# Kernel tuning notes

Measured on AMD Instinct MI355X. Metric: run time of the kernel, lower is better.

Reference implementation:

```python
import jax, jax.numpy as jnp
import numpy as np


def _patch_desc(x, patch_size):
    # x: (n, c, h, w). Replicate-pad by patch_size//2 and gather all
    # patch_size*patch_size shifted views -> (n, c*p*p, h*w) descriptors.
    n, c, h, w = x.shape
    step = patch_size // 2
    y = jnp.pad(x, ((0, 0), (0, 0), (step, step), (step, step)), mode='edge')
    feats = [y[:, :, i:i + h, j:j + w]
             for i in range(patch_size) for j in range(patch_size)]
    d = jnp.stack(feats, axis=2)            # (n, c, p*p, h, w)
    return d.reshape(n, c * patch_size * patch_size, h * w)


def setup_inputs() -> dict:
    key = jax.random.key(0)
    k1, k2 = jax.random.split(key)
    n, c, h, w = 4, 16, 64, 64
    s = jax.random.normal(k1, (n, c, h, w), dtype=jnp.float32)
    t = jax.random.normal(k2, (n, c, h, w), dtype=jnp.float32)
    return {"s": s, "t": t, "patch_size": 3}


def reference(s, t, patch_size):
    n, c, h, w = s.shape
    q = _patch_desc(s, patch_size)          # (n, d, hw) source queries
    p = _patch_desc(t, patch_size)          # (n, d, hw) target points
    # Squared-L2 nearest neighbor per source patch (exact version of FLANN kNN)
    qn = jnp.sum(q * q, axis=1)             # (n, hw)
    pn = jnp.sum(p * p, axis=1)             # (n, hw)
    cross = jnp.einsum('ndi,ndj->nij', q, p)  # (n, hw_q, hw_t)
    d2 = qn[:, :, None] - 2.0 * cross + pn[:, None, :]
    idx = jnp.argmin(d2, axis=2)            # (n, hw) flat target index
    nnd = jnp.min(d2, axis=2)               # (n, hw) squared distance
    idy = idx // w
    idx_x = idx % w
    nnf = jnp.stack([idy.reshape(n, h, w), idx_x.reshape(n, h, w)], axis=1)
    nnd = nnd.reshape(n, 1, h, w)
    return nnf.astype(jnp.int32), nnd
```

## Files before the change

kernel.cpp:

```cpp
#include <hip/hip_runtime.h>


#define N_  4
#define C_  16
#define H_  64
#define W_  64
#define HW_ 4096
#define KK_ 18
#define SPLITS_M 4
#define KKSTRIDE 512

#define SPLITS_V 4
#define TILES_PER_SPLIT_V 4

typedef _Float16 f16;
typedef _Float16 f16x8 __attribute__((ext_vector_type(8)));
typedef float    f32x4 __attribute__((ext_vector_type(4)));
typedef float    f32x16 __attribute__((ext_vector_type(16)));

__device__ __forceinline__ int iclamp(int v, int lo, int hi) {
    return v < lo ? lo : (v > hi ? hi : v);
}

__device__ __forceinline__ void async_ld16(const void* g, void* l) {
    __builtin_amdgcn_global_load_lds(
        (const __attribute__((address_space(1))) unsigned int*)g,
        (__attribute__((address_space(3))) unsigned int*)l, 16, 0, 0);
}

__global__ __launch_bounds__(256)
void build_desc_norms_kernel(const float* __restrict__ s,
                             const float* __restrict__ t,
                             f16* __restrict__ Qh, f16* __restrict__ Ql,
                             f16* __restrict__ Ph, f16* __restrict__ Pl,
                             float* __restrict__ pn,
                             float* __restrict__ qn) {
    const int y0  = blockIdx.x;
    const int n   = blockIdx.y;
    const int src = blockIdx.z;
    const float* img = (src ? s : t) + n * (C_ * HW_);
    f16* Dh = src ? Qh : Ph;
    f16* Dl = src ? Ql : Pl;
    float* nrm = src ? qn : pn;

    __shared__ float imgS[3][C_][W_];
    __shared__ float nS[4][W_];
    const int tid = threadIdx.x;
    #pragma unroll
    for (int k = 0; k < 12; ++k) {
        const int idx = tid + k * 256;
        const int x = idx & 63, c = (idx >> 6) & 15, r = idx >> 10;
        const int gy = iclamp(y0 + r - 1, 0, H_ - 1);
        imgS[r][c][x] = img[c * HW_ + gy * W_ + x];
    }
    __syncthreads();

    const int q = tid >> 6, x = tid & 63;
    const int pix = y0 * W_ + x;
    float nacc = 0.f;
    #pragma unroll
    for (int u = 0; u < 5; ++u) {
        const int kk = q * 5 + u;
        if (kk < KK_) {
            f16x8 hv, lv;
            const int d  = kk >> 1;
            const int c0 = (kk & 1) * 8;
            const int dy = (d * 11) >> 5;
            const int dx = d - dy * 3;
            const int xs = iclamp(x + dx - 1, 0, W_ - 1);
            #pragma unroll
            for (int cc = 0; cc < 8; ++cc) {
                const float v = imgS[dy][c0 + cc][xs];
                const f16 h = (f16)v;
                hv[cc] = h;
                lv[cc] = (f16)(v - (float)h);
                nacc += v * v;
            }
            const size_t off = ((size_t)(n * KK_ + kk) * HW_ + pix) * 8;
            *(f16x8*)&Dh[off] = hv;
            *(f16x8*)&Dl[off] = lv;
        }
    }
    nS[q][x] = nacc;
    __syncthreads();
    if (tid < W_)
        nrm[n * HW_ + pix] = nS[0][tid] + nS[1][tid] + nS[2][tid] + nS[3][tid];
}

__global__ __launch_bounds__(256, 2)
void mfma_nn_kernel(const f16* __restrict__ Qh, const f16* __restrict__ Ql,
                    const f16* __restrict__ Ph, const f16* __restrict__ Pl,
                    const float* __restrict__ pn_g,
                    unsigned long long* __restrict__ partial) {
    const int bid   = blockIdx.x;
    const int split = bid & 3;
    const int n     = (bid >> 2) & 3;
    const int iblk  = bid >> 4;
    const int tid  = threadIdx.x;
    const int wave = tid >> 6, lane = tid & 63;
    const int col  = lane & 31;
    const int half = lane >> 5;
    const int irow0 = iblk * 128 + wave * 32;

    __shared__ f16 Bbuf[4][KK_ * KKSTRIDE];
    __shared__ float pnS[1024];

    f16x8 Ah[9], Al[9];
    #pragma unroll
    for (int c = 0; c < 9; ++c) {
        const size_t off = ((size_t)(n * KK_ + 2 * c + half) * HW_ +
                            irow0 + col) * 8;
        Ah[c] = *(const f16x8*)(Qh + off);
        Al[c] = *(const f16x8*)(Ql + off);
    }

    const int jsplit0 = split * 1024;
    #pragma unroll
    for (int k = 0; k < 4; ++k)
        pnS[tid + k * 256] = pn_g[n * HW_ + jsplit0 + tid + k * 256];

    float    bd[16];
    unsigned bj[16];
    #pragma unroll
    for (int r = 0; r < 16; ++r) { bd[r] = -3.0e38f; bj[r] = 0u; }

    const int stile = wave >> 1;
    const int skk0  = (wave & 1) * 9;
    const f16* sbase = half ? Pl : Ph;

    #define STAGE(PAIR, T0)                                                   \
        {   _Pragma("unroll")                                                 \
            for (int u = 0; u < 9; ++u) {                                     \
                const int kk = skk0 + u;                                      \
                const f16* g = sbase + ((size_t)(n * KK_ + kk) * HW_ +        \
                                        jsplit0 + ((T0) + stile) * 32 +       \
                                        col) * 8;                             \
                async_ld16(g, (void*)&Bbuf[(PAIR) * 2 + stile]                \
                                          [kk * KKSTRIDE + lane * 8]);        \
            }                                                                 \
        }

    #define BAR()                                                             \
        {   asm volatile("s_waitcnt vmcnt(0)" ::: "memory");                  \
            asm volatile("s_barrier" ::: "memory");                           \
        }

    #define COMPUTE2(PAIR, T0)                                                \
        {   const int j0 = (T0) * 32 + col;                                   \
            const float pnv0 = -0.5f * pnS[j0];                               \
            const float pnv1 = -0.5f * pnS[j0 + 32];                          \
            f32x16 C0, C1;                                                    \
            _Pragma("unroll")                                                 \
            for (int r = 0; r < 16; ++r) { C0[r] = pnv0; C1[r] = pnv1; }      \
            __builtin_amdgcn_s_setprio(1);                                    \
            _Pragma("unroll")                                                 \
            for (int c = 0; c < 9; ++c) {                                     \
                const int kb = (2 * c + half) * KKSTRIDE + col * 8;           \
                const f16x8 bh0 = *(const f16x8*)&Bbuf[(PAIR) * 2][kb];       \
                const f16x8 bl0 = *(const f16x8*)&Bbuf[(PAIR) * 2][kb + 256]; \
                const f16x8 bh1 = *(const f16x8*)&Bbuf[(PAIR) * 2 + 1][kb];   \
                const f16x8 bl1 = *(const f16x8*)&Bbuf[(PAIR) * 2 + 1]        \
                                                      [kb + 256];             \
                C0 = __builtin_amdgcn_mfma_f32_32x32x16_f16(                  \
                    Ah[c], bh0, C0, 0, 0, 0);                                 \
                C1 = __builtin_amdgcn_mfma_f32_32x32x16_f16(                  \
                    Ah[c], bh1, C1, 0, 0, 0);                                 \
                C0 = __builtin_amdgcn_mfma_f32_32x32x16_f16(                  \
                    Al[c], bh0, C0, 0, 0, 0);                                 \
                C1 = __builtin_amdgcn_mfma_f32_32x32x16_f16(                  \
                    Al[c], bh1, C1, 0, 0, 0);                                 \
                C0 = __builtin_amdgcn_mfma_f32_32x32x16_f16(                  \
                    Ah[c], bl0, C0, 0, 0, 0);                                 \
                C1 = __builtin_amdgcn_mfma_f32_32x32x16_f16(                  \
                    Ah[c], bl1, C1, 0, 0, 0);                                 \
            }                                                                 \
            __builtin_amdgcn_s_setprio(0);                                    \
            _Pragma("unroll")                                                 \
            for (int r = 0; r < 16; ++r) {                                    \
                if (C0[r] > bd[r]) { bd[r] = C0[r]; bj[r] = (unsigned)j0; }   \
                if (C1[r] > bd[r]) { bd[r] = C1[r];                           \
                                     bj[r] = (unsigned)(j0 + 32); }           \
            }                                                                 \
        }

    STAGE(0, 0)
    asm volatile("s_waitcnt vmcnt(0)" ::: "memory");
    __syncthreads();

    STAGE(1, 2)  COMPUTE2(0, 0)
    for (int gg = 0; gg < 6; ++gg) {
        const int t4 = gg * 4;
        BAR()  STAGE(0, t4 + 4)  COMPUTE2(1, t4 + 2)
        BAR()  STAGE(1, t4 + 6)  COMPUTE2(0, t4 + 4)
    }
    BAR()  STAGE(0, 28)  COMPUTE2(1, 26)
    BAR()  STAGE(1, 30)  COMPUTE2(0, 28)
    BAR()               COMPUTE2(1, 30)
    #undef STAGE
    #undef BAR
    #undef COMPUTE2

    #pragma unroll
    for (int r = 0; r < 16; ++r) {
        float    d = bd[r];
        unsigned j = (unsigned)jsplit0 + bj[r];
        #pragma unroll
        for (int off = 1; off < 32; off <<= 1) {
            const float    od = __shfl_xor(d, off, 64);
            const unsigned oj = __shfl_xor(j, off, 64);
            const bool take = (od > d) || (od == d && oj < j);
            d = take ? od : d;
            j = take ? oj : j;
        }
        if (col == 0) {
            const int i = irow0 + (r & 3) + 8 * (r >> 2) + 4 * half;
            partial[(size_t)(split * N_ + n) * HW_ + i] =
                ((unsigned long long)j << 32) |
                (unsigned long long)__float_as_uint(-2.f * d);
        }
    }
}

__global__ __launch_bounds__(256)
void finalize_mfma_kernel(const unsigned long long* __restrict__ partial,
                          const float* __restrict__ qn_g,
                          float* __restrict__ out) {
    const int id  = blockIdx.x * 256 + threadIdx.x;
    const int n   = id >> 12;
    const int pix = id & 4095;
    float    bd = 3.0e38f;
    unsigned bj = 0u;
    #pragma unroll
    for (int sp = 0; sp < SPLITS_M; ++sp) {
        const unsigned long long v = partial[(size_t)(sp * N_ + n) * HW_ + pix];
        const float    d = __uint_as_float((unsigned)(v & 0xffffffffull));
        const unsigned j = (unsigned)(v >> 32);
        const bool take = (d < bd) || (d == bd && j < bj);
        bd = take ? d : bd;
        bj = take ? j : bj;
    }
    out[n * 2 * HW_ + pix]            = (float)(bj >> 6);
    out[n * 2 * HW_ + HW_ + pix]      = (float)(bj & 63);
    out[N_ * 2 * HW_ + n * HW_ + pix] = bd + qn_g[n * HW_ + pix];
}

__global__ __launch_bounds__(256)
void prep_norms_kernel(const float* __restrict__ s,
                       const float* __restrict__ t,
                       float* __restrict__ pn,
                       float* __restrict__ qn) {
    const int gid   = blockIdx.x * 256 + threadIdx.x;
    const int which = gid >> 14;
    const int id    = gid & 16383;
    const int n     = id >> 12;
    const int pix   = id & 4095;
    const int y = pix >> 6, x = pix & 63;
    const float* base = (which ? s : t) + n * (C_ * HW_);
    float acc = 0.f;
    for (int c = 0; c < C_; ++c) {
        const float* bc = base + c * HW_;
        #pragma unroll
        for (int dy = 0; dy < 3; ++dy) {
            const float* br = bc + iclamp(y + dy - 1, 0, H_ - 1) * W_;
            #pragma unroll
            for (int dx = 0; dx < 3; ++dx) {
                float v = br[iclamp(x + dx - 1, 0, W_ - 1)];
                acc += v * v;
            }
        }
    }
    (which ? qn : pn)[id] = acc;
}

__global__ __launch_bounds__(256)
void patchmatch_main_kernel(const float* __restrict__ s,
                            const float* __restrict__ t,
                            const float* __restrict__ pn_g,
                            const float* __restrict__ qn_g,
                            unsigned long long* __restrict__ partial) {
    const int yq    = blockIdx.x;
    const int n     = blockIdx.y;
    const int split = blockIdx.z;
    const int tid  = threadIdx.x;
    const int tx   = tid & 15;
    const int ty   = tid >> 4;
    const int i0   = ty * 4;
    const int jrow = tx >> 2;
    const int jx0  = (tx & 3) * 16;

    __shared__ float qS[C_][3][68];
    __shared__ float tS[C_][6][68];
    __shared__ float qnS[W_];

    const float* sb = s + n * (C_ * HW_);
    const float* tb = t + n * (C_ * HW_);

    #pragma unroll
    for (int k = 0; k < 3; ++k) {
        const int id = tid + k * 256;
        const int sg = id & 15;
        const int c  = (id >> 4) & 15;
        const int r  = id >> 8;
        const int gr = iclamp(yq + r - 1, 0, H_ - 1);
        const float4 v = *(const float4*)&sb[c * HW_ + gr * W_ + sg * 4];
        float* dst = &qS[c][r][1 + sg * 4];
        dst[0] = v.x; dst[1] = v.y; dst[2] = v.z; dst[3] = v.w;
    }
    if (tid < 48) {
        const int c  = tid & 15;
        const int r  = tid >> 4;
        const int gr = iclamp(yq + r - 1, 0, H_ - 1);
        qS[c][r][0]  = sb[c * HW_ + gr * W_];
        qS[c][r][65] = sb[c * HW_ + gr * W_ + 63];
    }
    if (tid < W_) qnS[tid] = qn_g[n * HW_ + yq * W_ + tid];

    unsigned long long best[4] = {~0ull, ~0ull, ~0ull, ~0ull};

    for (int ytl = 0; ytl < TILES_PER_SPLIT_V; ++ytl) {
        const int yt = split * TILES_PER_SPLIT_V + ytl;
        __syncthreads();
        #pragma unroll
        for (int k = 0; k < 6; ++k) {
            const int id = tid + k * 256;
            const int sg = id & 15;
            const int c  = (id >> 4) & 15;
            const int r  = id >> 8;
            const int gr = iclamp(4 * yt + r - 1, 0, H_ - 1);
            const float4 v = *(const float4*)&tb[c * HW_ + gr * W_ + sg * 4];
            float* dst = &tS[c][r][1 + sg * 4];
            dst[0] = v.x; dst[1] = v.y; dst[2] = v.z; dst[3] = v.w;
        }
        if (tid < 96) {
            const int c  = tid & 15;
            const int r  = tid >> 4;
            const int gr = iclamp(4 * yt + r - 1, 0, H_ - 1);
            tS[c][r][0]  = tb[c * HW_ + gr * W_];
            tS[c][r][65] = tb[c * HW_ + gr * W_ + 63];
        }
        __syncthreads();

        float acc[4][16];
        #pragma unroll
        for (int a = 0; a < 4; ++a)
            #pragma unroll
            for (int b = 0; b < 16; ++b) acc[a][b] = 0.f;

        for (int c = 0; c < C_; ++c) {
            #pragma unroll
            for (int dy = 0; dy < 3; ++dy) {
                float qv[6], tv[18];
                *(float4*)&qv[0] = *(const float4*)&qS[c][dy][i0];
                *(float2*)&qv[4] = *(const float2*)&qS[c][dy][i0 + 4];
                const float* trow = &tS[c][jrow + dy][jx0];
                *(float4*)&tv[0]  = *(const float4*)&trow[0];
                *(float4*)&tv[4]  = *(const float4*)&trow[4];
                *(float4*)&tv[8]  = *(const float4*)&trow[8];
                *(float4*)&tv[12] = *(const float4*)&trow[12];
                *(float2*)&tv[16] = *(const float2*)&trow[16];
                #pragma unroll
                for (int dx = 0; dx < 3; ++dx)
                    #pragma unroll
                    for (int a = 0; a < 4; ++a)
                        #pragma unroll
                        for (int b = 0; b < 16; ++b)
                            acc[a][b] += qv[a + dx] * tv[b + dx];
            }
        }

        const int jbase = yt * 256 + jrow * W_ + jx0;
        float pnv[16];
        const float* png = &pn_g[n * HW_ + jbase];
        *(float4*)&pnv[0]  = *(const float4*)&png[0];
        *(float4*)&pnv[4]  = *(const float4*)&png[4];
        *(float4*)&pnv[8]  = *(const float4*)&png[8];
        *(float4*)&pnv[12] = *(const float4*)&png[12];
        #pragma unroll
        for (int a = 0; a < 4; ++a) {
            const float qn = qnS[i0 + a];
            #pragma unroll
            for (int b = 0; b < 16; ++b) {
                const float d2 = qn + pnv[b] - 2.f * acc[a][b];
                unsigned long long cand =
                    ((unsigned long long)__float_as_uint(d2) << 32) |
                    (unsigned)(jbase + b);
                best[a] = cand < best[a] ? cand : best[a];
            }
        }
    }

    #pragma unroll
    for (int a = 0; a < 4; ++a) {
        unsigned long long v = best[a];
        #pragma unroll
        for (int mm = 8; mm >= 1; mm >>= 1) {
            unsigned long long o = __shfl_xor(v, mm, 64);
            v = o < v ? o : v;
        }
        best[a] = v;
    }
    if (tx == 0) {
        #pragma unroll
        for (int a = 0; a < 4; ++a)
            partial[((split * N_ + n) * HW_) + yq * W_ + i0 + a] = best[a];
    }
}

__global__ __launch_bounds__(256)
void finalize_kernel(const unsigned long long* __restrict__ partial,
                     float* __restrict__ out) {
    const int id  = blockIdx.x * 256 + threadIdx.x;
    const int n   = id >> 12;
    const int pix = id & 4095;
    unsigned long long best = ~0ull;
    #pragma unroll
    for (int sp = 0; sp < SPLITS_V; ++sp) {
        unsigned long long v = partial[(sp * N_ + n) * HW_ + pix];
        best = v < best ? v : best;
    }
    const unsigned j = (unsigned)(best & 0xffffffffu);
    const float d2 = __uint_as_float((unsigned)(best >> 32));
    out[n * 2 * HW_ + pix]            = (float)(j >> 6);
    out[n * 2 * HW_ + HW_ + pix]      = (float)(j & 63);
    out[N_ * 2 * HW_ + n * HW_ + pix] = d2;
}

__global__ __launch_bounds__(256)
void patchmatch_mono_kernel(const float* __restrict__ s,
                            const float* __restrict__ t,
                            float* __restrict__ out) {
    const int yq  = blockIdx.x;
    const int n   = blockIdx.y;
    const int tid = threadIdx.x;
    const int tx  = tid & 15;
    const int ty  = tid >> 4;
    const int i0  = ty * 4;
    const int jrow = tx >> 3;
    const int jx0  = (tx & 7) * 8;

    __shared__ float qS[C_][3][68];
    __shared__ float tS[C_][4][68];
    __shared__ float pnS[HW_];
    __shared__ float qnS[W_];

    const float* sb = s + n * (C_ * HW_);
    const float* tb = t + n * (C_ * HW_);

    for (int jj = tid; jj < HW_; jj += 256) {
        const int y = jj >> 6, x = jj & 63;
        float acc = 0.f;
        for (int c = 0; c < C_; ++c) {
            const float* tc = tb + c * HW_;
            #pragma unroll
            for (int dy = 0; dy < 3; ++dy) {
                const float* tr = tc + iclamp(y + dy - 1, 0, H_ - 1) * W_;
                #pragma unroll
                for (int dx = 0; dx < 3; ++dx) {
                    float v = tr[iclamp(x + dx - 1, 0, W_ - 1)];
                    acc += v * v;
                }
            }
        }
        pnS[jj] = acc;
    }
    for (int idx = tid; idx < C_ * 3 * 66; idx += 256) {
        const int c   = idx / (3 * 66);
        const int rem = idx - c * (3 * 66);
        const int rr  = rem / 66;
        const int xi  = rem - rr * 66;
        qS[c][rr][xi] = sb[c * HW_ + iclamp(yq + rr - 1, 0, H_ - 1) * W_ +
                           iclamp(xi - 1, 0, W_ - 1)];
    }
    __syncthreads();
    if (tid < W_) {
        float acc = 0.f;
        for (int c = 0; c < C_; ++c)
            #pragma unroll
            for (int dy = 0; dy < 3; ++dy)
                #pragma unroll
                for (int dx = 0; dx < 3; ++dx) {
                    float v = qS[c][dy][tid + dx];
                    acc += v * v;
                }
        qnS[tid] = acc;
    }

    unsigned long long best[4] = {~0ull, ~0ull, ~0ull, ~0ull};
    for (int yt = 0; yt < 32; ++yt) {
        __syncthreads();
        for (int idx = tid; idx < C_ * 4 * 66; idx += 256) {
            const int c   = idx / (4 * 66);
            const int rem = idx - c * (4 * 66);
            const int rr  = rem / 66;
            const int xi  = rem - rr * 66;
            tS[c][rr][xi] = tb[c * HW_ + iclamp(2 * yt + rr - 1, 0, H_ - 1) * W_ +
                               iclamp(xi - 1, 0, W_ - 1)];
        }
        __syncthreads();

        float acc[4][8];
        #pragma unroll
        for (int a = 0; a < 4; ++a)
            #pragma unroll
            for (int b = 0; b < 8; ++b) acc[a][b] = 0.f;

        for (int c = 0; c < C_; ++c) {
            #pragma unroll
            for (int dy = 0; dy < 3; ++dy) {
                float qv[8], tv[12];
                *(float4*)&qv[0] = *(const float4*)&qS[c][dy][i0];
                *(float4*)&qv[4] = *(const float4*)&qS[c][dy][i0 + 4];
                const float* trow = &tS[c][jrow + dy][jx0];
                *(float4*)&tv[0] = *(const float4*)&trow[0];
                *(float4*)&tv[4] = *(const float4*)&trow[4];
                *(float4*)&tv[8] = *(const float4*)&trow[8];
                #pragma unroll
                for (int dx = 0; dx < 3; ++dx)
                    #pragma unroll
                    for (int a = 0; a < 4; ++a)
                        #pragma unroll
                        for (int b = 0; b < 8; ++b)
                            acc[a][b] += qv[a + dx] * tv[b + dx];
            }
        }
        const int rbase = (2 * yt + jrow) * W_ + jx0;
        #pragma unroll
        for (int a = 0; a < 4; ++a) {
            const float qn = qnS[i0 + a];
            #pragma unroll
            for (int b = 0; b < 8; ++b) {
                const int j = rbase + b;
                const float d2 = qn + pnS[j] - 2.f * acc[a][b];
                unsigned long long cand =
                    ((unsigned long long)__float_as_uint(d2) << 32) | (unsigned)j;
                best[a] = cand < best[a] ? cand : best[a];
            }
        }
    }
    #pragma unroll
    for (int a = 0; a < 4; ++a) {
        unsigned long long v = best[a];
        #pragma unroll
        for (int mm = 8; mm >= 1; mm >>= 1) {
            unsigned long long o = __shfl_xor(v, mm, 64);
            v = o < v ? o : v;
        }
        best[a] = v;
    }
    if (tx == 0) {
        #pragma unroll
        for (int a = 0; a < 4; ++a) {
            const int x = i0 + a;
            const unsigned j = (unsigned)(best[a] & 0xffffffffu);
            const float d2 = __uint_as_float((unsigned)(best[a] >> 32));
            const int pix = yq * W_ + x;
            out[n * 2 * HW_ + pix]            = (float)(j >> 6);
            out[n * 2 * HW_ + HW_ + pix]      = (float)(j & 63);
            out[N_ * 2 * HW_ + n * HW_ + pix] = d2;
        }
    }
}

extern "C" void kernel_launch(void* const* d_in, const int* in_sizes, int n_in,
                              void* d_out, int out_size, void* d_ws, size_t ws_size,
                              hipStream_t stream) {
    const float* s = (const float*)d_in[0];
    const float* t = (const float*)d_in[1];
    float* out = (float*)d_out;

    const size_t norm_b  = (size_t)N_ * HW_ * 4;
    const size_t part_b  = (size_t)SPLITS_M * N_ * HW_ * 8;
    const size_t desc_b  = (size_t)N_ * HW_ * KK_ * 8 * 2;
    const size_t need_m  = 2 * norm_b + part_b + 4 * desc_b;

    if (ws_size >= need_m) {
        char* w = (char*)d_ws;
        float* pn = (float*)w;                       w += norm_b;
        float* qn = (float*)w;                       w += norm_b;
        unsigned long long* partial = (unsigned long long*)w; w += part_b;
        f16* Qh = (f16*)w;  w += desc_b;
        f16* Ql = (f16*)w;  w += desc_b;
        f16* Ph = (f16*)w;  w += desc_b;
        f16* Pl = (f16*)w;

        build_desc_norms_kernel<<<dim3(64, N_, 2), 256, 0, stream>>>(
            s, t, Qh, Ql, Ph, Pl, pn, qn);
        mfma_nn_kernel<<<512, 256, 0, stream>>>(Qh, Ql, Ph, Pl, pn, partial);
        finalize_mfma_kernel<<<64, 256, 0, stream>>>(partial, qn, out);
        return;
    }

    const size_t need_v = 2 * norm_b + (size_t)SPLITS_V * N_ * HW_ * 8;
    if (ws_size >= need_v) {
        float* pn = (float*)d_ws;
        float* qn = pn + N_ * HW_;
        unsigned long long* partial =
            (unsigned long long*)((char*)d_ws + 2 * norm_b);
        prep_norms_kernel<<<128, 256, 0, stream>>>(s, t, pn, qn);
        dim3 grid(H_, N_, SPLITS_V);
        patchmatch_main_kernel<<<grid, 256, 0, stream>>>(s, t, pn, qn, partial);
        finalize_kernel<<<64, 256, 0, stream>>>(partial, out);
        return;
    }

    dim3 grid(H_, N_);
    patchmatch_mono_kernel<<<grid, 256, 0, stream>>>(s, t, out);
}
```

Baseline: 124.4 us.

## Load B operand directly from global memory instead of LDS double-buffering

Removes the async global-to-LDS staging pipeline with its double buffer and per-step barriers. Each wave now reads its B fragments (high and low halves of the target descriptors) straight from global memory into registers inside the MFMA loop, unrolled by two. This frees a large shared-memory footprint and the barrier stalls. The cost is that the four waves of a block each re-read the same B tiles from global/L2, and global-load latency now sits directly in the MFMA loop with no explicit prefetch.

```diff
diff --git a/kernel.cpp b/kernel.cpp
--- a/kernel.cpp
+++ b/kernel.cpp
@@ -8,8 +8,6 @@
 #define HW_ 4096
 #define KK_ 18
 #define SPLITS_M 4
-#define KKSTRIDE 512
-
 #define SPLITS_V 4
 #define TILES_PER_SPLIT_V 4
 
@@ -20,12 +18,6 @@
 
 __device__ __forceinline__ int iclamp(int v, int lo, int hi) {
     return v < lo ? lo : (v > hi ? hi : v);
-}
-
-__device__ __forceinline__ void async_ld16(const void* g, void* l) {
-    __builtin_amdgcn_global_load_lds(
-        (const __attribute__((address_space(1))) unsigned int*)g,
-        (__attribute__((address_space(3))) unsigned int*)l, 16, 0, 0);
 }
 
 __global__ __launch_bounds__(256)
@@ -102,7 +94,6 @@
     const int half = lane >> 5;
     const int irow0 = iblk * 128 + wave * 32;
 
-    __shared__ f16 Bbuf[4][KK_ * KKSTRIDE];
     __shared__ float pnS[1024];
 
     f16x8 Ah[9], Al[9];
@@ -118,87 +109,48 @@
     #pragma unroll
     for (int k = 0; k < 4; ++k)
         pnS[tid + k * 256] = pn_g[n * HW_ + jsplit0 + tid + k * 256];
+    __syncthreads();
 
     float    bd[16];
     unsigned bj[16];
     #pragma unroll
     for (int r = 0; r < 16; ++r) { bd[r] = -3.0e38f; bj[r] = 0u; }
 
-    const int stile = wave >> 1;
-    const int skk0  = (wave & 1) * 9;
-    const f16* sbase = half ? Pl : Ph;
-
-    #define STAGE(PAIR, T0)                                                   \
-        {   _Pragma("unroll")                                                 \
-            for (int u = 0; u < 9; ++u) {                                     \
-                const int kk = skk0 + u;                                      \
-                const f16* g = sbase + ((size_t)(n * KK_ + kk) * HW_ +        \
-                                        jsplit0 + ((T0) + stile) * 32 +       \
-                                        col) * 8;                             \
-                async_ld16(g, (void*)&Bbuf[(PAIR) * 2 + stile]                \
-                                          [kk * KKSTRIDE + lane * 8]);        \
-            }                                                                 \
-        }
-
-    #define BAR()                                                             \
-        {   asm volatile("s_waitcnt vmcnt(0)" ::: "memory");                  \
-            asm volatile("s_barrier" ::: "memory");                           \
-        }
-
-    #define COMPUTE2(PAIR, T0)                                                \
-        {   const int j0 = (T0) * 32 + col;                                   \
-            const float pnv0 = -0.5f * pnS[j0];                               \
-            const float pnv1 = -0.5f * pnS[j0 + 32];                          \
-            f32x16 C0, C1;                                                    \
-            _Pragma("unroll")                                                 \
-            for (int r = 0; r < 16; ++r) { C0[r] = pnv0; C1[r] = pnv1; }      \
-            __builtin_amdgcn_s_setprio(1);                                    \
-            _Pragma("unroll")                                                 \
-            for (int c = 0; c < 9; ++c) {                                     \
-                const int kb = (2 * c + half) * KKSTRIDE + col * 8;           \
-                const f16x8 bh0 = *(const f16x8*)&Bbuf[(PAIR) * 2][kb];       \
-                const f16x8 bl0 = *(const f16x8*)&Bbuf[(PAIR) * 2][kb + 256]; \
-                const f16x8 bh1 = *(const f16x8*)&Bbuf[(PAIR) * 2 + 1][kb];   \
-                const f16x8 bl1 = *(const f16x8*)&Bbuf[(PAIR) * 2 + 1]        \
-                                                      [kb + 256];             \
-                C0 = __builtin_amdgcn_mfma_f32_32x32x16_f16(                  \
-                    Ah[c], bh0, C0, 0, 0, 0);                                 \
-                C1 = __builtin_amdgcn_mfma_f32_32x32x16_f16(                  \
-                    Ah[c], bh1, C1, 0, 0, 0);                                 \
-                C0 = __builtin_amdgcn_mfma_f32_32x32x16_f16(                  \
-                    Al[c], bh0, C0, 0, 0, 0);                                 \
-                C1 = __builtin_amdgcn_mfma_f32_32x32x16_f16(                  \
-                    Al[c], bh1, C1, 0, 0, 0);                                 \
-                C0 = __builtin_amdgcn_mfma_f32_32x32x16_f16(                  \
-                    Ah[c], bl0, C0, 0, 0, 0);                                 \
-                C1 = __builtin_amdgcn_mfma_f32_32x32x16_f16(                  \
-                    Ah[c], bl1, C1, 0, 0, 0);                                 \
-            }                                                                 \
-            __builtin_amdgcn_s_setprio(0);                                    \
-            _Pragma("unroll")                                                 \
-            for (int r = 0; r < 16; ++r) {                                    \
-                if (C0[r] > bd[r]) { bd[r] = C0[r]; bj[r] = (unsigned)j0; }   \
-                if (C1[r] > bd[r]) { bd[r] = C1[r];                           \
-                                     bj[r] = (unsigned)(j0 + 32); }           \
-            }                                                                 \
-        }
-
-    STAGE(0, 0)
-    asm volatile("s_waitcnt vmcnt(0)" ::: "memory");
-    __syncthreads();
-
-    STAGE(1, 2)  COMPUTE2(0, 0)
-    for (int gg = 0; gg < 6; ++gg) {
-        const int t4 = gg * 4;
-        BAR()  STAGE(0, t4 + 4)  COMPUTE2(1, t4 + 2)
-        BAR()  STAGE(1, t4 + 6)  COMPUTE2(0, t4 + 4)
-    }
-    BAR()  STAGE(0, 28)  COMPUTE2(1, 26)
-    BAR()  STAGE(1, 30)  COMPUTE2(0, 28)
-    BAR()               COMPUTE2(1, 30)
-    #undef STAGE
-    #undef BAR
-    #undef COMPUTE2
+    const f16* __restrict__ bhb =
+        Ph + ((size_t)(n * KK_ + half) * HW_ + jsplit0 + col) * 8;
+    const f16* __restrict__ blb =
+        Pl + ((size_t)(n * KK_ + half) * HW_ + jsplit0 + col) * 8;
+
+    #pragma unroll 2
+    for (int p = 0; p < 16; ++p) {
+        const int j0 = p * 64 + col;
+        const float pnv0 = -0.5f * pnS[j0];
+        const float pnv1 = -0.5f * pnS[j0 + 32];
+        f32x16 C0, C1;
+        #pragma unroll
+        for (int r = 0; r < 16; ++r) { C0[r] = pnv0; C1[r] = pnv1; }
+        const f16* ph = bhb + p * 512;
+        const f16* pl = blb + p * 512;
+        #pragma unroll
+        for (int c = 0; c < 9; ++c) {
+            const size_t co = (size_t)c * (2 * HW_ * 8);
+            const f16x8 bh0 = *(const f16x8*)(ph + co);
+            const f16x8 bh1 = *(const f16x8*)(ph + co + 256);
+            const f16x8 bl0 = *(const f16x8*)(pl + co);
+            const f16x8 bl1 = *(const f16x8*)(pl + co + 256);
+            C0 = __builtin_amdgcn_mfma_f32_32x32x16_f16(Ah[c], bh0, C0, 0, 0, 0);
+            C1 = __builtin_amdgcn_mfma_f32_32x32x16_f16(Ah[c], bh1, C1, 0, 0, 0);
+            C0 = __builtin_amdgcn_mfma_f32_32x32x16_f16(Al[c], bh0, C0, 0, 0, 0);
+            C1 = __builtin_amdgcn_mfma_f32_32x32x16_f16(Al[c], bh1, C1, 0, 0, 0);
+            C0 = __builtin_amdgcn_mfma_f32_32x32x16_f16(Ah[c], bl0, C0, 0, 0, 0);
+            C1 = __builtin_amdgcn_mfma_f32_32x32x16_f16(Ah[c], bl1, C1, 0, 0, 0);
+        }
+        #pragma unroll
+        for (int r = 0; r < 16; ++r) {
+            if (C0[r] > bd[r]) { bd[r] = C0[r]; bj[r] = (unsigned)j0; }
+            if (C1[r] > bd[r]) { bd[r] = C1[r]; bj[r] = (unsigned)(j0 + 32); }
+        }
+    }
 
     #pragma unroll
     for (int r = 0; r < 16; ++r) {
```

After: 136.4 us. +9.7%, slower.

## Fuse descriptor build, MFMA search and finalize into one cooperative kernel

Applied to the files above, without the earlier changes.

Adds a cooperative kernel that merges the three phases (descriptor/norm build, MFMA nearest-neighbor search, final reduction) and separates them with grid-wide syncs. This removes two kernel launch gaps. It also vectorizes the image loads into LDS with float4. The cost is grid barrier overhead and the constraint that all 512 blocks must be co-resident (2 per CU). If the occupancy check or the cooperative launch fails, it falls back to the old three-kernel path.

```diff
diff --git a/kernel.cpp b/kernel.cpp
--- a/kernel.cpp
+++ b/kernel.cpp
@@ -1,4 +1,5 @@
 #include <hip/hip_runtime.h>
+#include <hip/hip_cooperative_groups.h>
 
 
 #define N_  4
@@ -18,6 +19,8 @@
 typedef float    f32x4 __attribute__((ext_vector_type(4)));
 typedef float    f32x16 __attribute__((ext_vector_type(16)));
 
+namespace cg = cooperative_groups;
+
 __device__ __forceinline__ int iclamp(int v, int lo, int hi) {
     return v < lo ? lo : (v > hi ? hi : v);
 }
@@ -26,6 +29,234 @@
     __builtin_amdgcn_global_load_lds(
         (const __attribute__((address_space(1))) unsigned int*)g,
         (__attribute__((address_space(3))) unsigned int*)l, 16, 0, 0);
+}
+
+__global__ __launch_bounds__(256, 2)
+void fused_nn_kernel(const float* __restrict__ s, const float* __restrict__ t,
+                     f16* __restrict__ Qh, f16* __restrict__ Ql,
+                     f16* __restrict__ Ph, f16* __restrict__ Pl,
+                     float* __restrict__ pn, float* __restrict__ qn,
+                     unsigned long long* __restrict__ partial,
+                     float* __restrict__ out) {
+    cg::grid_group grid = cg::this_grid();
+
+    __shared__ __align__(16) f16 Bbuf[4][KK_ * KKSTRIDE];
+    __shared__ float pnS[1024];
+
+    const int bid = blockIdx.x;
+    const int tid = threadIdx.x;
+
+    {
+        const int y0  = bid & 63;
+        const int n   = (bid >> 6) & 3;
+        const int src = bid >> 8;
+        const float* img = (src ? s : t) + n * (C_ * HW_);
+        f16* Dh = src ? Qh : Ph;
+        f16* Dl = src ? Ql : Pl;
+        float* nrm = src ? qn : pn;
+
+        float (*imgS)[C_][W_] = (float (*)[C_][W_]) & Bbuf[0][0];
+        float (*nS)[W_] = (float (*)[W_])((char*)&Bbuf[0][0] + 12288);
+
+        #pragma unroll
+        for (int k = 0; k < 3; ++k) {
+            const int i4 = tid + k * 256;
+            const int x4 = i4 & 15, c = (i4 >> 4) & 15, r = i4 >> 8;
+            const int gy = iclamp(y0 + r - 1, 0, H_ - 1);
+            const float4 v = *(const float4*)&img[c * HW_ + gy * W_ + x4 * 4];
+            *(float4*)&imgS[r][c][x4 * 4] = v;
+        }
+        __syncthreads();
+
+        const int q = tid >> 6, x = tid & 63;
+        const int pix = y0 * W_ + x;
+        float nacc = 0.f;
+        #pragma unroll
+        for (int u = 0; u < 5; ++u) {
+            const int kk = q * 5 + u;
+            if (kk < KK_) {
+                f16x8 hv, lv;
+                const int d  = kk >> 1;
+                const int c0 = (kk & 1) * 8;
+                const int dy = (d * 11) >> 5;
+                const int dx = d - dy * 3;
+                const int xs = iclamp(x + dx - 1, 0, W_ - 1);
+                #pragma unroll
+                for (int cc = 0; cc < 8; ++cc) {
+                    const float v = imgS[dy][c0 + cc][xs];
+                    const f16 h = (f16)v;
+                    hv[cc] = h;
+                    lv[cc] = (f16)(v - (float)h);
+                    nacc += v * v;
+                }
+                const size_t off = ((size_t)(n * KK_ + kk) * HW_ + pix) * 8;
+                *(f16x8*)&Dh[off] = hv;
+                *(f16x8*)&Dl[off] = lv;
+            }
+        }
+        nS[q][x] = nacc;
+        __syncthreads();
+        if (tid < W_)
+            nrm[n * HW_ + pix] =
+                nS[0][tid] + nS[1][tid] + nS[2][tid] + nS[3][tid];
+    }
+
+    __threadfence();
+    grid.sync();
+    __threadfence();
+
+    {
+        const int split = bid & 3;
+        const int n     = (bid >> 2) & 3;
+        const int iblk  = bid >> 4;
+        const int wave = tid >> 6, lane = tid & 63;
+        const int col  = lane & 31;
+        const int half = lane >> 5;
+        const int irow0 = iblk * 128 + wave * 32;
+
+        f16x8 Ah[9], Al[9];
+        #pragma unroll
+        for (int c = 0; c < 9; ++c) {
+            const size_t off = ((size_t)(n * KK_ + 2 * c + half) * HW_ +
+                                irow0 + col) * 8;
+            Ah[c] = *(const f16x8*)(Qh + off);
+            Al[c] = *(const f16x8*)(Ql + off);
+        }
+
+        const int jsplit0 = split * 1024;
+        #pragma unroll
+        for (int k = 0; k < 4; ++k)
+            pnS[tid + k * 256] = pn[n * HW_ + jsplit0 + tid + k * 256];
+
+        float    bd[16];
+        unsigned bj[16];
+        #pragma unroll
+        for (int r = 0; r < 16; ++r) { bd[r] = -3.0e38f; bj[r] = 0u; }
+
+        const int stile = wave >> 1;
+        const int skk0  = (wave & 1) * 9;
+        const f16* sbase = half ? Pl : Ph;
+
+        #define STAGE(PAIR, T0)                                               \
+            {   _Pragma("unroll")                                             \
+                for (int u = 0; u < 9; ++u) {                                 \
+                    const int kk = skk0 + u;                                  \
+                    const f16* g = sbase + ((size_t)(n * KK_ + kk) * HW_ +    \
+                                            jsplit0 + ((T0) + stile) * 32 +   \
+                                            col) * 8;                         \
+                    async_ld16(g, (void*)&Bbuf[(PAIR) * 2 + stile]            \
+                                              [kk * KKSTRIDE + lane * 8]);    \
+                }                                                             \
+            }
+
+        #define BAR()                                                         \
+            {   asm volatile("s_waitcnt vmcnt(0)" ::: "memory");              \
+                asm volatile("s_barrier" ::: "memory");                       \
+            }
+
+        #define COMPUTE2(PAIR, T0)                                            \
+            {   const int j0 = (T0) * 32 + col;                               \
+                const float pnv0 = -0.5f * pnS[j0];                           \
+                const float pnv1 = -0.5f * pnS[j0 + 32];                      \
+                f32x16 C0, C1;                                                \
+                _Pragma("unroll")                                             \
+                for (int r = 0; r < 16; ++r) { C0[r] = pnv0; C1[r] = pnv1; }  \
+                __builtin_amdgcn_s_setprio(1);                                \
+                _Pragma("unroll")                                             \
+                for (int c = 0; c < 9; ++c) {                                 \
+                    const int kb = (2 * c + half) * KKSTRIDE + col * 8;       \
+                    const f16x8 bh0 = *(const f16x8*)&Bbuf[(PAIR) * 2][kb];   \
+                    const f16x8 bl0 = *(const f16x8*)&Bbuf[(PAIR) * 2]        \
+                                                          [kb + 256];         \
+                    const f16x8 bh1 = *(const f16x8*)&Bbuf[(PAIR) * 2 + 1]    \
+                                                          [kb];               \
+                    const f16x8 bl1 = *(const f16x8*)&Bbuf[(PAIR) * 2 + 1]    \
+                                                          [kb + 256];         \
+                    C0 = __builtin_amdgcn_mfma_f32_32x32x16_f16(              \
+                        Ah[c], bh0, C0, 0, 0, 0);                             \
+                    C1 = __builtin_amdgcn_mfma_f32_32x32x16_f16(              \
+                        Ah[c], bh1, C1, 0, 0, 0);                             \
+                    C0 = __builtin_amdgcn_mfma_f32_32x32x16_f16(              \
+                        Al[c], bh0, C0, 0, 0, 0);                             \
+                    C1 = __builtin_amdgcn_mfma_f32_32x32x16_f16(              \
+                        Al[c], bh1, C1, 0, 0, 0);                             \
+                    C0 = __builtin_amdgcn_mfma_f32_32x32x16_f16(              \
+                        Ah[c], bl0, C0, 0, 0, 0);                             \
+                    C1 = __builtin_amdgcn_mfma_f32_32x32x16_f16(              \
+                        Ah[c], bl1, C1, 0, 0, 0);                             \
+                }                                                             \
+                __builtin_amdgcn_s_setprio(0);                                \
+                _Pragma("unroll")                                             \
+                for (int r = 0; r < 16; ++r) {                                \
+                    if (C0[r] > bd[r]) { bd[r] = C0[r];                       \
+                                         bj[r] = (unsigned)j0; }              \
+                    if (C1[r] > bd[r]) { bd[r] = C1[r];                       \
+                                         bj[r] = (unsigned)(j0 + 32); }       \
+                }                                                             \
+            }
+
+        STAGE(0, 0)
+        asm volatile("s_waitcnt vmcnt(0)" ::: "memory");
+        __syncthreads();
+
+        STAGE(1, 2)  COMPUTE2(0, 0)
+        for (int gg = 0; gg < 6; ++gg) {
+            const int t4 = gg * 4;
+            BAR()  STAGE(0, t4 + 4)  COMPUTE2(1, t4 + 2)
+            BAR()  STAGE(1, t4 + 6)  COMPUTE2(0, t4 + 4)
+        }
+        BAR()  STAGE(0, 28)  COMPUTE2(1, 26)
+        BAR()  STAGE(1, 30)  COMPUTE2(0, 28)
+        BAR()               COMPUTE2(1, 30)
+        #undef STAGE
+        #undef BAR
+        #undef COMPUTE2
+
+        #pragma unroll
+        for (int r = 0; r < 16; ++r) {
+            float    d = bd[r];
+            unsigned j = (unsigned)jsplit0 + bj[r];
+            #pragma unroll
+            for (int off = 1; off < 32; off <<= 1) {
+                const float    od = __shfl_xor(d, off, 64);
+                const unsigned oj = __shfl_xor(j, off, 64);
+                const bool take = (od > d) || (od == d && oj < j);
+                d = take ? od : d;
+                j = take ? oj : j;
+            }
+            if (col == 0) {
+                const int i = irow0 + (r & 3) + 8 * (r >> 2) + 4 * half;
+                partial[(size_t)(split * N_ + n) * HW_ + i] =
+                    ((unsigned long long)j << 32) |
+                    (unsigned long long)__float_as_uint(-2.f * d);
+            }
+        }
+    }
+
+    __threadfence();
+    grid.sync();
+    __threadfence();
+
+    if (tid < 32) {
+        const int id  = bid * 32 + tid;
+        const int n   = id >> 12;
+        const int pix = id & 4095;
+        float    fbd = 3.0e38f;
+        unsigned fbj = 0u;
+        #pragma unroll
+        for (int sp = 0; sp < SPLITS_M; ++sp) {
+            const unsigned long long v =
+                partial[(size_t)(sp * N_ + n) * HW_ + pix];
+            const float    d = __uint_as_float((unsigned)(v & 0xffffffffull));
+            const unsigned j = (unsigned)(v >> 32);
+            const bool take = (d < fbd) || (d == fbd && j < fbj);
+            fbd = take ? d : fbd;
+            fbj = take ? j : fbj;
+        }
+        out[n * 2 * HW_ + pix]            = (float)(fbj >> 6);
+        out[n * 2 * HW_ + HW_ + pix]      = (float)(fbj & 63);
+        out[N_ * 2 * HW_ + n * HW_ + pix] = fbd + qn[n * HW_ + pix];
+    }
 }
 
 __global__ __launch_bounds__(256)
@@ -47,11 +278,12 @@
     __shared__ float nS[4][W_];
     const int tid = threadIdx.x;
     #pragma unroll
-    for (int k = 0; k < 12; ++k) {
-        const int idx = tid + k * 256;
-        const int x = idx & 63, c = (idx >> 6) & 15, r = idx >> 10;
+    for (int k = 0; k < 3; ++k) {
+        const int i4 = tid + k * 256;
+        const int x4 = i4 & 15, c = (i4 >> 4) & 15, r = i4 >> 8;
         const int gy = iclamp(y0 + r - 1, 0, H_ - 1);
-        imgS[r][c][x] = img[c * HW_ + gy * W_ + x];
+        const float4 v = *(const float4*)&img[c * HW_ + gy * W_ + x4 * 4];
+        *(float4*)&imgS[r][c][x4 * 4] = v;
     }
     __syncthreads();
 
@@ -583,6 +815,24 @@
         f16* Ph = (f16*)w;  w += desc_b;
         f16* Pl = (f16*)w;
 
+        static int coop_state = -1;
+        if (coop_state == -1) {
+            int nb = 0;
+            hipError_t qe = hipOccupancyMaxActiveBlocksPerMultiprocessor(
+                &nb, fused_nn_kernel, 256, 0);
+            coop_state = (qe == hipSuccess && nb >= 2) ? 1 : 0;
+        }
+        if (coop_state == 1) {
+            void* args[] = {(void*)&s, (void*)&t, (void*)&Qh, (void*)&Ql,
+                            (void*)&Ph, (void*)&Pl, (void*)&pn, (void*)&qn,
+                            (void*)&partial, (void*)&out};
+            hipError_t le = hipLaunchCooperativeKernel(
+                (const void*)fused_nn_kernel, dim3(512), dim3(256),
+                args, 0, stream);
+            if (le == hipSuccess) return;
+            coop_state = 0;
+        }
+
         build_desc_norms_kernel<<<dim3(64, N_, 2), 256, 0, stream>>>(
             s, t, Qh, Ql, Ph, Pl, pn, qn);
         mfma_nn_kernel<<<512, 256, 0, stream>>>(Qh, Ql, Ph, Pl, pn, partial);
```

New measurement: 125.6 us. Within noise of the previous version (+1.0%).

## Fuse query descriptor build and finalize into MFMA kernel via atomic-min reduction

Applied to the files above, without the earlier changes.

The query descriptors (hi/lo f16 split) and query norms are now built inside the MFMA kernel from the source image staged in LDS, so the Q descriptor buffers and their global round trip go away. The separate finalize kernel is replaced by a 64-bit atomicMin on an order-preserving key plus a per-block counter, and the last-arriving split block writes the output. The target build uses float4 loads. This removes one kernel launch and the Q write/read traffic, at the cost of two memset launches, atomics and extra prologue work in every MFMA block, with Q rebuilt redundantly by each of the four splits.

```diff
diff --git a/kernel.cpp b/kernel.cpp
--- a/kernel.cpp
+++ b/kernel.cpp
@@ -29,29 +29,23 @@
 }
 
 __global__ __launch_bounds__(256)
-void build_desc_norms_kernel(const float* __restrict__ s,
-                             const float* __restrict__ t,
-                             f16* __restrict__ Qh, f16* __restrict__ Ql,
-                             f16* __restrict__ Ph, f16* __restrict__ Pl,
-                             float* __restrict__ pn,
-                             float* __restrict__ qn) {
-    const int y0  = blockIdx.x;
-    const int n   = blockIdx.y;
-    const int src = blockIdx.z;
-    const float* img = (src ? s : t) + n * (C_ * HW_);
-    f16* Dh = src ? Qh : Ph;
-    f16* Dl = src ? Ql : Pl;
-    float* nrm = src ? qn : pn;
+void build_P_kernel(const float* __restrict__ t,
+                    f16* __restrict__ Ph, f16* __restrict__ Pl,
+                    float* __restrict__ pn) {
+    const int y0 = blockIdx.x;
+    const int n  = blockIdx.y;
+    const float* img = t + n * (C_ * HW_);
 
     __shared__ float imgS[3][C_][W_];
     __shared__ float nS[4][W_];
     const int tid = threadIdx.x;
     #pragma unroll
-    for (int k = 0; k < 12; ++k) {
-        const int idx = tid + k * 256;
-        const int x = idx & 63, c = (idx >> 6) & 15, r = idx >> 10;
+    for (int k = 0; k < 3; ++k) {
+        const int i4 = tid + k * 256;
+        const int x4 = i4 & 15, c = (i4 >> 4) & 15, r = i4 >> 8;
         const int gy = iclamp(y0 + r - 1, 0, H_ - 1);
-        imgS[r][c][x] = img[c * HW_ + gy * W_ + x];
+        const float4 v = *(const float4*)&img[c * HW_ + gy * W_ + x4 * 4];
+        *(float4*)&imgS[r][c][x4 * 4] = v;
     }
     __syncthreads();
 
@@ -77,21 +71,23 @@
                 nacc += v * v;
             }
             const size_t off = ((size_t)(n * KK_ + kk) * HW_ + pix) * 8;
-            *(f16x8*)&Dh[off] = hv;
-            *(f16x8*)&Dl[off] = lv;
+            *(f16x8*)&Ph[off] = hv;
+            *(f16x8*)&Pl[off] = lv;
         }
     }
     nS[q][x] = nacc;
     __syncthreads();
     if (tid < W_)
-        nrm[n * HW_ + pix] = nS[0][tid] + nS[1][tid] + nS[2][tid] + nS[3][tid];
+        pn[n * HW_ + pix] = nS[0][tid] + nS[1][tid] + nS[2][tid] + nS[3][tid];
 }
 
 __global__ __launch_bounds__(256, 2)
-void mfma_nn_kernel(const f16* __restrict__ Qh, const f16* __restrict__ Ql,
+void mfma_nn_kernel(const float* __restrict__ s,
                     const f16* __restrict__ Ph, const f16* __restrict__ Pl,
                     const float* __restrict__ pn_g,
-                    unsigned long long* __restrict__ partial) {
+                    unsigned long long* __restrict__ best,
+                    unsigned* __restrict__ cnt,
+                    float* __restrict__ out) {
     const int bid   = blockIdx.x;
     const int split = bid & 3;
     const int n     = (bid >> 2) & 3;
@@ -102,146 +98,178 @@
     const int half = lane >> 5;
     const int irow0 = iblk * 128 + wave * 32;
 
-    __shared__ f16 Bbuf[4][KK_ * KKSTRIDE];
+    __shared__ __align__(16) f16 Bbuf[4][KK_ * KKSTRIDE];
     __shared__ float pnS[1024];
-
-    f16x8 Ah[9], Al[9];
-    #pragma unroll
-    for (int c = 0; c < 9; ++c) {
-        const size_t off = ((size_t)(n * KK_ + 2 * c + half) * HW_ +
-                            irow0 + col) * 8;
-        Ah[c] = *(const f16x8*)(Qh + off);
-        Al[c] = *(const f16x8*)(Ql + off);
-    }
+    __shared__ int lastFlag;
 
     const int jsplit0 = split * 1024;
     #pragma unroll
     for (int k = 0; k < 4; ++k)
         pnS[tid + k * 256] = pn_g[n * HW_ + jsplit0 + tid + k * 256];
 
-    float    bd[16];
-    unsigned bj[16];
-    #pragma unroll
-    for (int r = 0; r < 16; ++r) { bd[r] = -3.0e38f; bj[r] = 0u; }
-
-    const int stile = wave >> 1;
-    const int skk0  = (wave & 1) * 9;
-    const f16* sbase = half ? Pl : Ph;
-
-    #define STAGE(PAIR, T0)                                                   \
-        {   _Pragma("unroll")                                                 \
-            for (int u = 0; u < 9; ++u) {                                     \
-                const int kk = skk0 + u;                                      \
-                const f16* g = sbase + ((size_t)(n * KK_ + kk) * HW_ +        \
-                                        jsplit0 + ((T0) + stile) * 32 +       \
-                                        col) * 8;                             \
-                async_ld16(g, (void*)&Bbuf[(PAIR) * 2 + stile]                \
-                                          [kk * KKSTRIDE + lane * 8]);        \
-            }                                                                 \
-        }
-
-    #define BAR()                                                             \
-        {   asm volatile("s_waitcnt vmcnt(0)" ::: "memory");                  \
-            asm volatile("s_barrier" ::: "memory");                           \
-        }
-
-    #define COMPUTE2(PAIR, T0)                                                \
-        {   const int j0 = (T0) * 32 + col;                                   \
-            const float pnv0 = -0.5f * pnS[j0];                               \
-            const float pnv1 = -0.5f * pnS[j0 + 32];                          \
-            f32x16 C0, C1;                                                    \
-            _Pragma("unroll")                                                 \
-            for (int r = 0; r < 16; ++r) { C0[r] = pnv0; C1[r] = pnv1; }      \
-            __builtin_amdgcn_s_setprio(1);                                    \
-            _Pragma("unroll")                                                 \
-            for (int c = 0; c < 9; ++c) {                                     \
-                const int kb = (2 * c + half) * KKSTRIDE + col * 8;           \
-                const f16x8 bh0 = *(const f16x8*)&Bbuf[(PAIR) * 2][kb];       \
-                const f16x8 bl0 = *(const f16x8*)&Bbuf[(PAIR) * 2][kb + 256]; \
-                const f16x8 bh1 = *(const f16x8*)&Bbuf[(PAIR) * 2 + 1][kb];   \
-                const f16x8 bl1 = *(const f16x8*)&Bbuf[(PAIR) * 2 + 1]        \
-                                                      [kb + 256];             \
-                C0 = __builtin_amdgcn_mfma_f32_32x32x16_f16(                  \
-                    Ah[c], bh0, C0, 0, 0, 0);                                 \
-                C1 = __builtin_amdgcn_mfma_f32_32x32x16_f16(                  \
-                    Ah[c], bh1, C1, 0, 0, 0);                                 \
-                C0 = __builtin_amdgcn_mfma_f32_32x32x16_f16(                  \
-                    Al[c], bh0, C0, 0, 0, 0);                                 \
-                C1 = __builtin_amdgcn_mfma_f32_32x32x16_f16(                  \
-                    Al[c], bh1, C1, 0, 0, 0);                                 \
-                C0 = __builtin_amdgcn_mfma_f32_32x32x16_f16(                  \
-                    Ah[c], bl0, C0, 0, 0, 0);                                 \
-                C1 = __builtin_amdgcn_mfma_f32_32x32x16_f16(                  \
-                    Ah[c], bl1, C1, 0, 0, 0);                                 \
-            }                                                                 \
-            __builtin_amdgcn_s_setprio(0);                                    \
-            _Pragma("unroll")                                                 \
-            for (int r = 0; r < 16; ++r) {                                    \
-                if (C0[r] > bd[r]) { bd[r] = C0[r]; bj[r] = (unsigned)j0; }   \
-                if (C1[r] > bd[r]) { bd[r] = C1[r];                           \
-                                     bj[r] = (unsigned)(j0 + 32); }           \
-            }                                                                 \
-        }
-
-    STAGE(0, 0)
-    asm volatile("s_waitcnt vmcnt(0)" ::: "memory");
-    __syncthreads();
-
-    STAGE(1, 2)  COMPUTE2(0, 0)
-    for (int gg = 0; gg < 6; ++gg) {
-        const int t4 = gg * 4;
-        BAR()  STAGE(0, t4 + 4)  COMPUTE2(1, t4 + 2)
-        BAR()  STAGE(1, t4 + 6)  COMPUTE2(0, t4 + 4)
-    }
-    BAR()  STAGE(0, 28)  COMPUTE2(1, 26)
-    BAR()  STAGE(1, 30)  COMPUTE2(0, 28)
-    BAR()               COMPUTE2(1, 30)
-    #undef STAGE
-    #undef BAR
-    #undef COMPUTE2
-
-    #pragma unroll
-    for (int r = 0; r < 16; ++r) {
-        float    d = bd[r];
-        unsigned j = (unsigned)jsplit0 + bj[r];
-        #pragma unroll
-        for (int off = 1; off < 32; off <<= 1) {
-            const float    od = __shfl_xor(d, off, 64);
-            const unsigned oj = __shfl_xor(j, off, 64);
-            const bool take = (od > d) || (od == d && oj < j);
-            d = take ? od : d;
-            j = take ? oj : j;
-        }
-        if (col == 0) {
-            const int i = irow0 + (r & 3) + 8 * (r >> 2) + 4 * half;
-            partial[(size_t)(split * N_ + n) * HW_ + i] =
-                ((unsigned long long)j << 32) |
-                (unsigned long long)__float_as_uint(-2.f * d);
-        }
-    }
-}
-
-__global__ __launch_bounds__(256)
-void finalize_mfma_kernel(const unsigned long long* __restrict__ partial,
-                          const float* __restrict__ qn_g,
-                          float* __restrict__ out) {
-    const int id  = blockIdx.x * 256 + threadIdx.x;
-    const int n   = id >> 12;
-    const int pix = id & 4095;
-    float    bd = 3.0e38f;
-    unsigned bj = 0u;
-    #pragma unroll
-    for (int sp = 0; sp < SPLITS_M; ++sp) {
-        const unsigned long long v = partial[(size_t)(sp * N_ + n) * HW_ + pix];
-        const float    d = __uint_as_float((unsigned)(v & 0xffffffffull));
-        const unsigned j = (unsigned)(v >> 32);
-        const bool take = (d < bd) || (d == bd && j < bj);
-        bd = take ? d : bd;
-        bj = take ? j : bj;
-    }
-    out[n * 2 * HW_ + pix]            = (float)(bj >> 6);
-    out[n * 2 * HW_ + HW_ + pix]      = (float)(bj & 63);
-    out[N_ * 2 * HW_ + n * HW_ + pix] = bd + qn_g[n * HW_ + pix];
+    {
+        float (*imgS)[C_][W_] = (float (*)[C_][W_]) & Bbuf[0][0];
+        const float* simg = s + n * (C_ * HW_);
+        const int r0 = iblk * 2;
+        #pragma unroll
+        for (int k = 0; k < 4; ++k) {
+            const int i4 = tid + k * 256;
+            const int x4 = i4 & 15, c = (i4 >> 4) & 15, r = i4 >> 8;
+            const int gy = iclamp(r0 + r - 1, 0, H_ - 1);
+            const float4 v = *(const float4*)&simg[c * HW_ + gy * W_ + x4 * 4];
+            *(float4*)&imgS[r][c][x4 * 4] = v;
+        }
+        __syncthreads();
+
+        const int yloc = wave >> 1;
+        const int x    = (wave & 1) * 32 + col;
+        float nq = 0.f;
+        f16x8 Ah[9], Al[9];
+        #pragma unroll
+        for (int c = 0; c < 9; ++c) {
+            const int dy = (c * 11) >> 5;
+            const int dx = c - dy * 3;
+            const int xs = iclamp(x + dx - 1, 0, W_ - 1);
+            const int rr = yloc + dy;
+            #pragma unroll
+            for (int cc = 0; cc < 8; ++cc) {
+                const float v = imgS[rr][half * 8 + cc][xs];
+                const f16 h = (f16)v;
+                Ah[c][cc] = h;
+                Al[c][cc] = (f16)(v - (float)h);
+                nq += v * v;
+            }
+        }
+        nq += __shfl_xor(nq, 32, 64);
+        __syncthreads();
+
+        float    bd[16];
+        unsigned bj[16];
+        #pragma unroll
+        for (int r = 0; r < 16; ++r) { bd[r] = -3.0e38f; bj[r] = 0u; }
+
+        const int stile = wave >> 1;
+        const int skk0  = (wave & 1) * 9;
+        const f16* sbase = half ? Pl : Ph;
+
+        #define STAGE(PAIR, T0)                                               \
+            {   _Pragma("unroll")                                             \
+                for (int u = 0; u < 9; ++u) {                                 \
+                    const int kk = skk0 + u;                                  \
+                    const f16* g = sbase + ((size_t)(n * KK_ + kk) * HW_ +    \
+                                            jsplit0 + ((T0) + stile) * 32 +   \
+                                            col) * 8;                         \
+                    async_ld16(g, (void*)&Bbuf[(PAIR) * 2 + stile]            \
+                                              [kk * KKSTRIDE + lane * 8]);    \
+                }                                                             \
+            }
+
+        #define BAR()                                                         \
+            {   asm volatile("s_waitcnt vmcnt(0)" ::: "memory");              \
+                asm volatile("s_barrier" ::: "memory");                       \
+            }
+
+        #define COMPUTE2(PAIR, T0)                                            \
+            {   const int j0 = (T0) * 32 + col;                               \
+                const float pnv0 = -0.5f * pnS[j0];                           \
+                const float pnv1 = -0.5f * pnS[j0 + 32];                      \
+                f32x16 C0, C1;                                                \
+                _Pragma("unroll")                                             \
+                for (int r = 0; r < 16; ++r) { C0[r] = pnv0; C1[r] = pnv1; }  \
+                __builtin_amdgcn_s_setprio(1);                                \
+                _Pragma("unroll")                                             \
+                for (int c = 0; c < 9; ++c) {                                 \
+                    const int kb = (2 * c + half) * KKSTRIDE + col * 8;       \
+                    const f16x8 bh0 = *(const f16x8*)&Bbuf[(PAIR) * 2][kb];   \
+                    const f16x8 bl0 = *(const f16x8*)&Bbuf[(PAIR) * 2]        \
+                                                          [kb + 256];         \
+                    const f16x8 bh1 = *(const f16x8*)&Bbuf[(PAIR) * 2 + 1]    \
+                                                          [kb];               \
+                    const f16x8 bl1 = *(const f16x8*)&Bbuf[(PAIR) * 2 + 1]    \
+                                                          [kb + 256];         \
+                    C0 = __builtin_amdgcn_mfma_f32_32x32x16_f16(              \
+                        Ah[c], bh0, C0, 0, 0, 0);                             \
+                    C1 = __builtin_amdgcn_mfma_f32_32x32x16_f16(              \
+                        Ah[c], bh1, C1, 0, 0, 0);                             \
+                    C0 = __builtin_amdgcn_mfma_f32_32x32x16_f16(              \
+                        Al[c], bh0, C0, 0, 0, 0);                             \
+                    C1 = __builtin_amdgcn_mfma_f32_32x32x16_f16(              \
+                        Al[c], bh1, C1, 0, 0, 0);                             \
+                    C0 = __builtin_amdgcn_mfma_f32_32x32x16_f16(              \
+                        Ah[c], bl0, C0, 0, 0, 0);                             \
+                    C1 = __builtin_amdgcn_mfma_f32_32x32x16_f16(              \
+                        Ah[c], bl1, C1, 0, 0, 0);                             \
+                }                                                             \
+                __builtin_amdgcn_s_setprio(0);                                \
+                _Pragma("unroll")                                             \
+                for (int r = 0; r < 16; ++r) {                                \
+                    if (C0[r] > bd[r]) { bd[r] = C0[r];                       \
+                                         bj[r] = (unsigned)j0; }              \
+                    if (C1[r] > bd[r]) { bd[r] = C1[r];                       \
+                                         bj[r] = (unsigned)(j0 + 32); }       \
+                }                                                             \
+            }
+
+        STAGE(0, 0)
+        asm volatile("s_waitcnt vmcnt(0)" ::: "memory");
+        __syncthreads();
+
+        STAGE(1, 2)  COMPUTE2(0, 0)
+        for (int gg = 0; gg < 6; ++gg) {
+            const int t4 = gg * 4;
+            BAR()  STAGE(0, t4 + 4)  COMPUTE2(1, t4 + 2)
+            BAR()  STAGE(1, t4 + 6)  COMPUTE2(0, t4 + 4)
+        }
+        BAR()  STAGE(0, 28)  COMPUTE2(1, 26)
+        BAR()  STAGE(1, 30)  COMPUTE2(0, 28)
+        BAR()               COMPUTE2(1, 30)
+        #undef STAGE
+        #undef BAR
+        #undef COMPUTE2
+
+        #pragma unroll
+        for (int r = 0; r < 16; ++r) {
+            float    d = bd[r];
+            unsigned j = (unsigned)jsplit0 + bj[r];
+            #pragma unroll
+            for (int off = 1; off < 32; off <<= 1) {
+                const float    od = __shfl_xor(d, off, 64);
+                const unsigned oj = __shfl_xor(j, off, 64);
+                const bool take = (od > d) || (od == d && oj < j);
+                d = take ? od : d;
+                j = take ? oj : j;
+            }
+            if (col == 0) {
+                const int i = irow0 + (r & 3) + 8 * (r >> 2) + 4 * half;
+                unsigned ub = __float_as_uint(-2.f * d);
+                ub = (ub & 0x80000000u) ? ~ub : (ub | 0x80000000u);
+                const unsigned long long key =
+                    ((unsigned long long)ub << 32) | (unsigned long long)j;
+                atomicMin(&best[(size_t)n * HW_ + i], key);
+            }
+        }
+
+        __syncthreads();
+        if (tid == 0) {
+            __threadfence();
+            const unsigned old = atomicAdd(&cnt[n * 32 + iblk], 1u);
+            lastFlag = (old == SPLITS_M - 1);
+        }
+        __syncthreads();
+
+        if (lastFlag && half == 0) {
+            const int i = irow0 + col;
+            const size_t gi = (size_t)n * HW_ + i;
+            const unsigned long long v = atomicOr(&best[gi], 0ull);
+            const unsigned j = (unsigned)(v & 0xffffffffu);
+            unsigned ub = (unsigned)(v >> 32);
+            ub = (ub & 0x80000000u) ? (ub & 0x7fffffffu) : ~ub;
+            out[(size_t)n * 2 * HW_ + i]           = (float)(j >> 6);
+            out[(size_t)n * 2 * HW_ + HW_ + i]     = (float)(j & 63);
+            out[(size_t)N_ * 2 * HW_ + (size_t)n * HW_ + i] =
+                __uint_as_float(ub) + nq;
+        }
+    }
 }
 
 __global__ __launch_bounds__(256)
@@ -568,25 +596,24 @@
     const float* t = (const float*)d_in[1];
     float* out = (float*)d_out;
 
-    const size_t norm_b  = (size_t)N_ * HW_ * 4;
-    const size_t part_b  = (size_t)SPLITS_M * N_ * HW_ * 8;
-    const size_t desc_b  = (size_t)N_ * HW_ * KK_ * 8 * 2;
-    const size_t need_m  = 2 * norm_b + part_b + 4 * desc_b;
+    const size_t norm_b = (size_t)N_ * HW_ * 4;
+    const size_t best_b = (size_t)N_ * HW_ * 8;
+    const size_t cnt_b  = 4096;
+    const size_t desc_b = (size_t)N_ * HW_ * KK_ * 8 * 2;
+    const size_t need_m = norm_b + best_b + cnt_b + 2 * desc_b;
 
     if (ws_size >= need_m) {
         char* w = (char*)d_ws;
         float* pn = (float*)w;                       w += norm_b;
-        float* qn = (float*)w;                       w += norm_b;
-        unsigned long long* partial = (unsigned long long*)w; w += part_b;
-        f16* Qh = (f16*)w;  w += desc_b;
-        f16* Ql = (f16*)w;  w += desc_b;
+        unsigned long long* best = (unsigned long long*)w; w += best_b;
+        unsigned* cnt = (unsigned*)w;                w += cnt_b;
         f16* Ph = (f16*)w;  w += desc_b;
         f16* Pl = (f16*)w;
 
-        build_desc_norms_kernel<<<dim3(64, N_, 2), 256, 0, stream>>>(
-            s, t, Qh, Ql, Ph, Pl, pn, qn);
-        mfma_nn_kernel<<<512, 256, 0, stream>>>(Qh, Ql, Ph, Pl, pn, partial);
-        finalize_mfma_kernel<<<64, 256, 0, stream>>>(partial, qn, out);
+        hipMemsetAsync(best, 0xFF, best_b, stream);
+        hipMemsetAsync(cnt, 0, (size_t)N_ * 32 * 4, stream);
+        build_P_kernel<<<dim3(64, N_), 256, 0, stream>>>(t, Ph, Pl, pn);
+        mfma_nn_kernel<<<512, 256, 0, stream>>>(s, Ph, Pl, pn, best, cnt, out);
         return;
     }
 
```

Result: no change. 126.7 us (+1.9%).
